# Kernel tuning notes

Hardware: AMD Instinct MI355X
Metric: run time of the kernel (lower is better)

The kernel has to match this reference:

```python
import jax, jax.numpy as jnp
import numpy as np

N = 65536   # num nodes
F = 512     # input feature dim
H = 256     # hid_dim
E = 1048576 # num edges (avg degree 16)
R = 512     # num_reps


def setup_inputs() -> dict:
    key = jax.random.key(0)
    ks = jax.random.split(key, 8)
    nodes = jax.random.normal(ks[0], (N, F), dtype=jnp.float32)
    c_nodes = jax.random.normal(ks[1], (N, F), dtype=jnp.float32)  # corrupted features
    senders = jax.random.randint(ks[2], (E,), 0, N, dtype=jnp.int32)
    receivers = jax.random.randint(ks[3], (E,), 0, N, dtype=jnp.int32)
    s = 1.0 / np.sqrt(F)
    W = jax.random.uniform(ks[4], (F, H), jnp.float32, -s, s)  # Dense kernel
    b = jnp.zeros((H,), jnp.float32)                            # Dense bias
    W_bilinear = jax.random.normal(ks[5], (H, H), jnp.float32) / np.sqrt(H)
    centers = jax.random.normal(ks[6], (R, H), jnp.float32)     # EucCluster param
    return dict(nodes=nodes, c_nodes=c_nodes, senders=senders, receivers=receivers,
                W=W, b=b, W_bilinear=W_bilinear, centers=centers)


def _gcn(x, senders, receivers, W, b):
    # jraph.GraphConvolution(Dense, add_self_edges=False, symmetric_normalization=True)
    x = x @ W + b  # [N,H]
    ones = jnp.ones((senders.shape[0],), x.dtype)
    deg_s = jax.ops.segment_sum(ones, senders, num_segments=N)
    x = x * jax.lax.rsqrt(jnp.maximum(deg_s, 1.0))[:, None]
    x = jax.ops.segment_sum(x[senders], receivers, num_segments=N)  # scatter-sum aggregation
    deg_r = jax.ops.segment_sum(ones, receivers, num_segments=N)
    x = x * jax.lax.rsqrt(jnp.maximum(deg_r, 1.0))[:, None]
    return jax.nn.selu(x)  # activation 'SeLU'


def reference(nodes, c_nodes, senders, receivers, W, b, W_bilinear, centers):
    # DGI with shared single-layer GCN (train=False path; single layer => no dropout)
    nodes1 = _gcn(nodes, senders, receivers, W, b)    # [N,H]
    nodes2 = _gcn(c_nodes, senders, receivers, W, b)  # [N,H]
    summary = jax.nn.sigmoid(jnp.mean(nodes1, axis=0))  # dgi_readout, [H]
    all_nodes = jnp.concatenate([nodes1, nodes2], axis=0)  # [2N,H]
    logits = (all_nodes @ W_bilinear) @ summary  # bilinear, [2N]
    # row L2-normalize embeddings
    emb = nodes1 / jnp.linalg.norm(nodes1, axis=1, keepdims=True)
    # Euclidean clustering: pairwise dists via GEMM trick
    d2 = (jnp.sum(emb * emb, axis=1)[:, None]
          + jnp.sum(centers * centers, axis=1)[None, :]
          - 2.0 * emb @ centers.T)  # [N,R]
    dists = jnp.sqrt(jnp.maximum(d2, 1e-12))
    cluster_dists = jnp.min(dists, axis=1)   # per-node dist to nearest center
    rep_ids = jnp.argmin(dists, axis=0)      # representative node per center
    cluster_loss = jnp.sum(cluster_dists)
    return emb, centers, rep_ids, cluster_loss, logits
```

## Files before the change

kernel.cpp:

```cpp
#include <hip/hip_runtime.h>
#include <math.h>

#define N_NODES 65536
#define F_DIM 512
#define H_DIM 256
#define E_EDGES 1048576
#define R_REPS 512

typedef _Float16 f16x8 __attribute__((ext_vector_type(8)));
typedef float f32x4_t __attribute__((ext_vector_type(4)));

__device__ __forceinline__ float selu_f(float x) {
    const float SC = 1.0507009873554804934f;
    const float AL = 1.6732632423543772848f;
    return x > 0.f ? SC * x : SC * AL * expm1f(x);
}

__device__ __forceinline__ void split8(const float* __restrict__ g, f16x8* hi, f16x8* lo) {
    float4 v0 = *(const float4*)g;
    float4 v1 = *(const float4*)(g + 4);
    f16x8 h, l;
    h[0] = (_Float16)v0.x; h[1] = (_Float16)v0.y; h[2] = (_Float16)v0.z; h[3] = (_Float16)v0.w;
    h[4] = (_Float16)v1.x; h[5] = (_Float16)v1.y; h[6] = (_Float16)v1.z; h[7] = (_Float16)v1.w;
    l[0] = (_Float16)(v0.x - (float)h[0]); l[1] = (_Float16)(v0.y - (float)h[1]);
    l[2] = (_Float16)(v0.z - (float)h[2]); l[3] = (_Float16)(v0.w - (float)h[3]);
    l[4] = (_Float16)(v1.x - (float)h[4]); l[5] = (_Float16)(v1.y - (float)h[5]);
    l[6] = (_Float16)(v1.z - (float)h[6]); l[7] = (_Float16)(v1.w - (float)h[7]);
    *hi = h; *lo = l;
}

__device__ __forceinline__ int wave_sort64(int v, int lane) {
    #pragma unroll
    for (int k = 2; k <= 64; k <<= 1) {
        #pragma unroll
        for (int j = k >> 1; j > 0; j >>= 1) {
            int p = __shfl_xor(v, j);
            bool takeMin = (((lane & j) == 0) == ((lane & k) == 0));
            int mn = min(v, p), mx = max(v, p);
            v = takeMin ? mn : mx;
        }
    }
    return v;
}

__global__ void k_init(int* cnt_s, int* cnt_r, float* colsum,
                       unsigned* node_min, unsigned long long* center_min,
                       double* loss_acc) {
    int i = blockIdx.x * 256 + threadIdx.x;
    if (i < N_NODES) { cnt_s[i] = 0; cnt_r[i] = 0; node_min[i] = 0x7F800000u; }
    if (i < H_DIM) colsum[i] = 0.f;
    if (i < R_REPS) center_min[i] = ~0ull;
    if (i == 0) *loss_acc = 0.0;
}

__global__ void k_degree(const int* __restrict__ senders, const int* __restrict__ receivers,
                         int* __restrict__ cnt_s, int* __restrict__ cnt_r) {
    int e = blockIdx.x * 256 + threadIdx.x;
    if (e < E_EDGES) {
        atomicAdd(&cnt_s[senders[e]], 1);
        atomicAdd(&cnt_r[receivers[e]], 1);
    }
}

__global__ void k_invsqrt(const int* __restrict__ cnt_s, const int* __restrict__ cnt_r,
                          float* __restrict__ inv_s, float* __restrict__ inv_r) {
    int i = blockIdx.x * 256 + threadIdx.x;
    if (i < N_NODES) {
        inv_s[i] = 1.0f / sqrtf(fmaxf((float)cnt_s[i], 1.f));
        inv_r[i] = 1.0f / sqrtf(fmaxf((float)cnt_r[i], 1.f));
    }
}

__global__ __launch_bounds__(1024) void k_scan(const int* __restrict__ cnt,
                                               int* __restrict__ row_ptr,
                                               int* __restrict__ cursor) {
    __shared__ int part[1024];
    int t = threadIdx.x;
    int base = t * 64;
    int s = 0;
    #pragma unroll 8
    for (int i = 0; i < 64; ++i) s += cnt[base + i];
    part[t] = s;
    __syncthreads();
    for (int off = 1; off < 1024; off <<= 1) {
        int other = (t >= off) ? part[t - off] : 0;
        __syncthreads();
        part[t] += other;
        __syncthreads();
    }
    int run = part[t] - s;
    for (int i = 0; i < 64; ++i) {
        row_ptr[base + i] = run;
        cursor[base + i] = run;
        run += cnt[base + i];
    }
    if (t == 1023) row_ptr[N_NODES] = run;
}

__global__ void k_fill(const int* __restrict__ senders, const int* __restrict__ receivers,
                       int* __restrict__ cursor, int* __restrict__ csr_send) {
    int e = blockIdx.x * 256 + threadIdx.x;
    if (e < E_EDGES) {
        int pos = atomicAdd(&cursor[receivers[e]], 1);
        csr_send[pos] = senders[e];
    }
}

__global__ void k_splitWT(const float* __restrict__ W, _Float16* __restrict__ hiT,
                          _Float16* __restrict__ loT) {
    int idx = blockIdx.x * 256 + threadIdx.x;
    int n = idx & (H_DIM - 1);
    int k = idx >> 8;
    float x = W[(size_t)k * H_DIM + n];
    _Float16 h = (_Float16)x;
    hiT[(size_t)n * F_DIM + k] = h;
    loT[(size_t)n * F_DIM + k] = (_Float16)(x - (float)h);
}

#define MFMA3(accv, AH, AL, BH, BL) \
    accv = __builtin_amdgcn_mfma_f32_16x16x32_f16(AH, BH, accv, 0, 0, 0); \
    accv = __builtin_amdgcn_mfma_f32_16x16x32_f16(AH, BL, accv, 0, 0, 0); \
    accv = __builtin_amdgcn_mfma_f32_16x16x32_f16(AL, BH, accv, 0, 0, 0);

#define MFMA_CORE \
    f16x8 ah[4], al[4]; \
    _Pragma("unroll") \
    for (int mi = 0; mi < 4; ++mi) { \
        ah[mi] = *(f16x8*)&Ah[wm * 64 + mi * 16 + lrow][kg * 8]; \
        al[mi] = *(f16x8*)&Al[wm * 64 + mi * 16 + lrow][kg * 8]; \
    } \
    _Pragma("unroll") \
    for (int ni = 0; ni < 4; ++ni) { \
        f16x8 bh = *(f16x8*)&Bh[wn * 64 + ni * 16 + lrow][kg * 8]; \
        f16x8 bl = *(f16x8*)&Bl[wn * 64 + ni * 16 + lrow][kg * 8]; \
        _Pragma("unroll") \
        for (int mi = 0; mi < 4; ++mi) { MFMA3(acc[mi][ni], ah[mi], al[mi], bh, bl) } \
    }

#define STAGE_A_F32(gA) { \
    f16x8 h0, l0, h1, l1; \
    split8((gA) + k0, &h0, &l0); \
    split8((gA) + k0 + 8, &h1, &l1); \
    *(f16x8*)&Ah[sr][skh] = h0; *(f16x8*)&Ah[sr][skh + 8] = h1; \
    *(f16x8*)&Al[sr][skh] = l0; *(f16x8*)&Al[sr][skh + 8] = l1; }

#define STAGE_B_F32(gB) { \
    f16x8 h0, l0, h1, l1; \
    split8((gB) + k0, &h0, &l0); \
    split8((gB) + k0 + 8, &h1, &l1); \
    *(f16x8*)&Bh[sr][skh] = h0; *(f16x8*)&Bh[sr][skh + 8] = h1; \
    *(f16x8*)&Bl[sr][skh] = l0; *(f16x8*)&Bl[sr][skh + 8] = l1; }

__global__ __launch_bounds__(256) void k_gemm_mfma(
    const float* __restrict__ A,
    const _Float16* __restrict__ BThi, const _Float16* __restrict__ BTlo,
    const float* __restrict__ bias, const float* __restrict__ inv_s,
    float* __restrict__ X, int K) {
    __shared__ _Float16 Ah[128][40], Al[128][40], Bh[128][40], Bl[128][40];
    const int t = threadIdx.x;
    const int lane = t & 63;
    const int wm = (t >> 6) >> 1, wn = (t >> 6) & 1;
    const int lrow = lane & 15, kg = lane >> 4;
    const int m0 = blockIdx.x * 128, n0 = blockIdx.y * 128;
    const int sr = t >> 1, skh = (t & 1) << 4;
    const float* gA = A + (size_t)(m0 + sr) * K + skh;
    const _Float16* gBh = BThi + (size_t)(n0 + sr) * K + skh;
    const _Float16* gBl = BTlo + (size_t)(n0 + sr) * K + skh;
    f32x4_t acc[4][4] = {};
    for (int k0 = 0; k0 < K; k0 += 32) {
        __syncthreads();
        STAGE_A_F32(gA)
        *(float4*)&Bh[sr][skh]     = *(const float4*)(gBh + k0);
        *(float4*)&Bh[sr][skh + 8] = *(const float4*)(gBh + k0 + 8);
        *(float4*)&Bl[sr][skh]     = *(const float4*)(gBl + k0);
        *(float4*)&Bl[sr][skh + 8] = *(const float4*)(gBl + k0 + 8);
        __syncthreads();
        MFMA_CORE
    }
    #pragma unroll
    for (int ni = 0; ni < 4; ++ni) {
        int col = n0 + wn * 64 + ni * 16 + lrow;
        float bc = bias[col];
        #pragma unroll
        for (int mi = 0; mi < 4; ++mi) {
            #pragma unroll
            for (int j = 0; j < 4; ++j) {
                int row = m0 + wm * 64 + mi * 16 + kg * 4 + j;
                X[(size_t)row * H_DIM + col] = (acc[mi][ni][j] + bc) * inv_s[row];
            }
        }
    }
}

__global__ __launch_bounds__(256) void k_cluster_mfma(
    const float* __restrict__ emb, const float* __restrict__ centers,
    const float* __restrict__ e2, const float* __restrict__ c2,
    unsigned* __restrict__ node_min, unsigned long long* __restrict__ center_min) {
    __shared__ _Float16 Ah[128][40], Al[128][40], Bh[128][40], Bl[128][40];
    __shared__ unsigned s_nmin[128];
    __shared__ unsigned long long s_cmin[128];
    const int t = threadIdx.x;
    const int lane = t & 63;
    const int wm = (t >> 6) >> 1, wn = (t >> 6) & 1;
    const int lrow = lane & 15, kg = lane >> 4;
    const int m0 = blockIdx.x * 128, n0 = blockIdx.y * 128;
    const int sr = t >> 1, skh = (t & 1) << 4;
    const int K = H_DIM;
    const float* gA = emb + (size_t)(m0 + sr) * K + skh;
    const float* gB = centers + (size_t)(n0 + sr) * K + skh;
    if (t < 128) { s_nmin[t] = 0x7F800000u; s_cmin[t] = ~0ull; }
    f32x4_t acc[4][4] = {};
    for (int k0 = 0; k0 < K; k0 += 32) {
        __syncthreads();
        STAGE_A_F32(gA)
        STAGE_B_F32(gB)
        __syncthreads();
        MFMA_CORE
    }
    float cv[4];
    #pragma unroll
    for (int ni = 0; ni < 4; ++ni) cv[ni] = c2[n0 + wn * 64 + ni * 16 + lrow];
    unsigned long long cb[4] = {~0ull, ~0ull, ~0ull, ~0ull};
    #pragma unroll
    for (int mi = 0; mi < 4; ++mi) {
        #pragma unroll
        for (int j = 0; j < 4; ++j) {
            int lr = wm * 64 + mi * 16 + kg * 4 + j;
            int row = m0 + lr;
            float ev = e2[row];
            float rmin = 3.402823466e+38f;
            #pragma unroll
            for (int ni = 0; ni < 4; ++ni) {
                float d2 = ev + cv[ni] - 2.f * acc[mi][ni][j];
                float d = sqrtf(fmaxf(d2, 1e-12f));
                rmin = fminf(rmin, d);
                unsigned long long pk = ((unsigned long long)__float_as_uint(d) << 32) | (unsigned)row;
                if (pk < cb[ni]) cb[ni] = pk;
            }
            atomicMin(&s_nmin[lr], __float_as_uint(rmin));
        }
    }
    #pragma unroll
    for (int ni = 0; ni < 4; ++ni)
        atomicMin(&s_cmin[wn * 64 + ni * 16 + lrow], cb[ni]);
    __syncthreads();
    if (t < 128) {
        atomicMin(&node_min[m0 + t], s_nmin[t]);
        atomicMin(&center_min[n0 + t], s_cmin[t]);
    }
}

__global__ __launch_bounds__(256) void k_agg1(
    const float* __restrict__ X, const int* __restrict__ csr_send,
    const int* __restrict__ row_ptr, const float* __restrict__ inv_r,
    float* __restrict__ out_emb) {
    int node = blockIdx.x * 4 + (threadIdx.x >> 6);
    int lane = threadIdx.x & 63;
    int beg = row_ptr[node], end = row_ptr[node + 1];
    float4 acc = {0.f, 0.f, 0.f, 0.f};
    for (int b = beg; b < end; b += 64) {
        int n = min(64, end - b);
        int myS = (lane < n) ? csr_send[b + lane] : 0x7FFFFFFF;
        myS = wave_sort64(myS, lane);
        for (int i = 0; i < n; ++i) {
            int s = __shfl(myS, i);
            float4 x = *(const float4*)&X[(size_t)s * H_DIM + (lane << 2)];
            acc.x += x.x; acc.y += x.y; acc.z += x.z; acc.w += x.w;
        }
    }
    float ir = inv_r[node];
    float4 o;
    o.x = selu_f(acc.x * ir);
    o.y = selu_f(acc.y * ir);
    o.z = selu_f(acc.z * ir);
    o.w = selu_f(acc.w * ir);
    *(float4*)&out_emb[(size_t)node * H_DIM + (lane << 2)] = o;
}

__global__ __launch_bounds__(256) void k_agg2(
    const float* __restrict__ X, const int* __restrict__ csr_send,
    const int* __restrict__ row_ptr, const float* __restrict__ inv_r,
    const float* __restrict__ v, float* __restrict__ out) {
    int node = blockIdx.x * 4 + (threadIdx.x >> 6);
    int lane = threadIdx.x & 63;
    int beg = row_ptr[node], end = row_ptr[node + 1];
    float4 acc = {0.f, 0.f, 0.f, 0.f};
    for (int b = beg; b < end; b += 64) {
        int n = min(64, end - b);
        int myS = (lane < n) ? csr_send[b + lane] : 0x7FFFFFFF;
        myS = wave_sort64(myS, lane);
        for (int i = 0; i < n; ++i) {
            int s = __shfl(myS, i);
            float4 x = *(const float4*)&X[(size_t)s * H_DIM + (lane << 2)];
            acc.x += x.x; acc.y += x.y; acc.z += x.z; acc.w += x.w;
        }
    }
    float ir = inv_r[node];
    float4 vv = *(const float4*)&v[lane << 2];
    float d = selu_f(acc.x * ir) * vv.x + selu_f(acc.y * ir) * vv.y
            + selu_f(acc.z * ir) * vv.z + selu_f(acc.w * ir) * vv.w;
    #pragma unroll
    for (int off = 32; off; off >>= 1) d += __shfl_down(d, off);
    if (lane == 0) out[node] = d;
}

__global__ __launch_bounds__(256) void k_colsum(const float* __restrict__ nodes1,
                                                float* __restrict__ colsum) {
    int t = threadIdx.x;
    size_t r0 = (size_t)blockIdx.x * 64;
    float s = 0.f;
    for (int r = 0; r < 64; ++r) s += nodes1[(r0 + r) * H_DIM + t];
    atomicAdd(&colsum[t], s);
}

__global__ void k_summary_v(const float* __restrict__ colsum, const float* __restrict__ Wb,
                            float* __restrict__ v) {
    __shared__ float s_sum[H_DIM];
    int t = threadIdx.x;
    float m = colsum[t] * (1.f / (float)N_NODES);
    s_sum[t] = 1.f / (1.f + expf(-m));
    __syncthreads();
    float acc = 0.f;
    for (int j = 0; j < H_DIM; ++j) acc += Wb[t * H_DIM + j] * s_sum[j];
    v[t] = acc;
}

__global__ __launch_bounds__(256) void k_normrow(
    float* __restrict__ emb, const float* __restrict__ v,
    float* __restrict__ logits, float* __restrict__ e2) {
    int row = blockIdx.x * 4 + (threadIdx.x >> 6);
    int lane = threadIdx.x & 63;
    float4 a = *(float4*)&emb[(size_t)row * H_DIM + (lane << 2)];
    float4 vv = *(const float4*)&v[lane << 2];
    float d = a.x * vv.x + a.y * vv.y + a.z * vv.z + a.w * vv.w;
    float ss = a.x * a.x + a.y * a.y + a.z * a.z + a.w * a.w;
    #pragma unroll
    for (int off = 32; off; off >>= 1) {
        d += __shfl_xor(d, off);
        ss += __shfl_xor(ss, off);
    }
    if (lane == 0) logits[row] = d;
    float inv = 1.f / sqrtf(ss);
    a.x *= inv; a.y *= inv; a.z *= inv; a.w *= inv;
    *(float4*)&emb[(size_t)row * H_DIM + (lane << 2)] = a;
    float s2 = a.x * a.x + a.y * a.y + a.z * a.z + a.w * a.w;
    #pragma unroll
    for (int off = 32; off; off >>= 1) s2 += __shfl_xor(s2, off);
    if (lane == 0) e2[row] = s2;
}

__global__ __launch_bounds__(256) void k_c2(const float* __restrict__ centers,
                                            float* __restrict__ c2) {
    int row = blockIdx.x * 4 + (threadIdx.x >> 6);
    int lane = threadIdx.x & 63;
    float4 a = *(const float4*)&centers[(size_t)row * H_DIM + (lane << 2)];
    float ss = a.x * a.x + a.y * a.y + a.z * a.z + a.w * a.w;
    #pragma unroll
    for (int off = 32; off; off >>= 1) ss += __shfl_xor(ss, off);
    if (lane == 0) c2[row] = ss;
}

__global__ __launch_bounds__(256) void k_loss(const unsigned* __restrict__ node_min,
                                              double* __restrict__ acc) {
    int i = blockIdx.x * 256 + threadIdx.x;
    float s = __uint_as_float(node_min[i]);
    #pragma unroll
    for (int off = 32; off; off >>= 1) s += __shfl_down(s, off);
    __shared__ float ws[4];
    int lane = threadIdx.x & 63, w = threadIdx.x >> 6;
    if (lane == 0) ws[w] = s;
    __syncthreads();
    if (threadIdx.x == 0) {
        float tot = ws[0] + ws[1] + ws[2] + ws[3];
        atomicAdd(acc, (double)tot);
    }
}

__global__ void k_finalize(const unsigned long long* __restrict__ center_min,
                           const double* __restrict__ loss_acc,
                           float* __restrict__ rep_out, float* __restrict__ loss_out) {
    int t = blockIdx.x * 256 + threadIdx.x;
    if (t < R_REPS) rep_out[t] = (float)(unsigned)(center_min[t] & 0xFFFFFFFFull);
    if (t == 0) *loss_out = (float)(*loss_acc);
}

extern "C" void kernel_launch(void* const* d_in, const int* in_sizes, int n_in,
                              void* d_out, int out_size, void* d_ws, size_t ws_size,
                              hipStream_t stream) {
    const float* nodes   = (const float*)d_in[0];
    const float* c_nodes = (const float*)d_in[1];
    const int* senders   = (const int*)d_in[2];
    const int* receivers = (const int*)d_in[3];
    const float* W       = (const float*)d_in[4];
    const float* bias    = (const float*)d_in[5];
    const float* Wb      = (const float*)d_in[6];
    const float* centers = (const float*)d_in[7];

    float* out = (float*)d_out;
    float* out_emb    = out;
    float* out_cent   = out + (size_t)N_NODES * H_DIM;
    float* out_rep    = out_cent + (size_t)R_REPS * H_DIM;
    float* out_loss   = out_rep + R_REPS;
    float* out_logits = out_loss + 1;

    char* wp = (char*)d_ws;
    unsigned long long* center_min = (unsigned long long*)wp; wp += (size_t)R_REPS * 8;
    double* loss_acc = (double*)wp;             wp += 8;
    float* X = (float*)wp;                      wp += (size_t)N_NODES * H_DIM * 4;
    int* csr_send = (int*)wp;                   wp += (size_t)E_EDGES * 4;
    int* row_ptr = (int*)wp;                    wp += (size_t)(N_NODES + 2) * 4;
    int* cursor = (int*)wp;                     wp += (size_t)N_NODES * 4;
    int* cnt_s = (int*)wp;                      wp += (size_t)N_NODES * 4;
    int* cnt_r = (int*)wp;                      wp += (size_t)N_NODES * 4;
    float* inv_s = (float*)wp;                  wp += (size_t)N_NODES * 4;
    float* inv_r = (float*)wp;                  wp += (size_t)N_NODES * 4;
    float* colsum = (float*)wp;                 wp += (size_t)H_DIM * 4;
    float* v = (float*)wp;                      wp += (size_t)H_DIM * 4;
    float* e2 = (float*)wp;                     wp += (size_t)N_NODES * 4;
    float* c2 = (float*)wp;                     wp += (size_t)R_REPS * 4;
    unsigned* node_min = (unsigned*)wp;         wp += (size_t)N_NODES * 4;
    _Float16* WhiT = (_Float16*)wp;             wp += (size_t)H_DIM * F_DIM * 2;
    _Float16* WloT = (_Float16*)wp;             wp += (size_t)H_DIM * F_DIM * 2;

    k_init<<<N_NODES / 256, 256, 0, stream>>>(cnt_s, cnt_r, colsum, node_min, center_min, loss_acc);
    k_degree<<<E_EDGES / 256, 256, 0, stream>>>(senders, receivers, cnt_s, cnt_r);
    k_invsqrt<<<N_NODES / 256, 256, 0, stream>>>(cnt_s, cnt_r, inv_s, inv_r);
    k_scan<<<1, 1024, 0, stream>>>(cnt_r, row_ptr, cursor);
    k_fill<<<E_EDGES / 256, 256, 0, stream>>>(senders, receivers, cursor, csr_send);
    k_splitWT<<<(F_DIM * H_DIM) / 256, 256, 0, stream>>>(W, WhiT, WloT);

    dim3 gg(N_NODES / 128, H_DIM / 128);
    k_gemm_mfma<<<gg, 256, 0, stream>>>(nodes, WhiT, WloT, bias, inv_s, X, F_DIM);
    k_agg1<<<N_NODES / 4, 256, 0, stream>>>(X, csr_send, row_ptr, inv_r, out_emb);

    k_colsum<<<N_NODES / 64, 256, 0, stream>>>(out_emb, colsum);
    k_summary_v<<<1, 256, 0, stream>>>(colsum, Wb, v);
    k_normrow<<<N_NODES / 4, 256, 0, stream>>>(out_emb, v, out_logits, e2);
    k_c2<<<R_REPS / 4, 256, 0, stream>>>(centers, c2);

    dim3 gc(N_NODES / 128, R_REPS / 128);
    k_cluster_mfma<<<gc, 256, 0, stream>>>(out_emb, centers, e2, c2, node_min, center_min);
    k_loss<<<N_NODES / 256, 256, 0, stream>>>(node_min, loss_acc);
    k_finalize<<<2, 256, 0, stream>>>(center_min, loss_acc, out_rep, out_loss);
    hipMemcpyAsync(out_cent, centers, (size_t)R_REPS * H_DIM * 4, hipMemcpyDeviceToDevice, stream);

    k_gemm_mfma<<<gg, 256, 0, stream>>>(c_nodes, WhiT, WloT, bias, inv_s, X, F_DIM);
    k_agg2<<<N_NODES / 4, 256, 0, stream>>>(X, csr_send, row_ptr, inv_r, v, out_logits + N_NODES);
}
```

Measured before the change: 902.2 us.

## Load GEMM B operands directly from global, batch both feature GEMMs

The two MFMA GEMM kernels no longer stage the B operand (split fp16 weights or centers) through shared memory. Each lane reads its fragments straight from global/L2, which halves LDS traffic and footprint per block. Centers are pre-split into hi/lo fp16 once, instead of being split per tile. Both node-feature GEMMs now run in one launch via blockIdx.z into separate buffers, and the grid is reordered so consecutive blocks share A rows. The cost is an extra N×H workspace buffer and uncoalesced, latency-exposed global loads for B inside the MFMA loop.

```diff
diff --git a/kernel.cpp b/kernel.cpp
--- a/kernel.cpp
+++ b/kernel.cpp
@@ -8,6 +8,7 @@
 #define R_REPS 512
 
 typedef _Float16 f16x8 __attribute__((ext_vector_type(8)));
+typedef _Float16 f16x4 __attribute__((ext_vector_type(4)));
 typedef float f32x4_t __attribute__((ext_vector_type(4)));
 
 __device__ __forceinline__ float selu_f(float x) {
@@ -117,12 +118,40 @@
     loT[(size_t)n * F_DIM + k] = (_Float16)(x - (float)h);
 }
 
+__global__ void k_split(const float* __restrict__ src, _Float16* __restrict__ hi,
+                        _Float16* __restrict__ lo, int n4) {
+    int i = blockIdx.x * 256 + threadIdx.x;
+    if (i >= n4) return;
+    float4 v = ((const float4*)src)[i];
+    f16x4 h, l;
+    h[0] = (_Float16)v.x; h[1] = (_Float16)v.y; h[2] = (_Float16)v.z; h[3] = (_Float16)v.w;
+    l[0] = (_Float16)(v.x - (float)h[0]);
+    l[1] = (_Float16)(v.y - (float)h[1]);
+    l[2] = (_Float16)(v.z - (float)h[2]);
+    l[3] = (_Float16)(v.w - (float)h[3]);
+    ((f16x4*)hi)[i] = h;
+    ((f16x4*)lo)[i] = l;
+}
+
 #define MFMA3(accv, AH, AL, BH, BL) \
     accv = __builtin_amdgcn_mfma_f32_16x16x32_f16(AH, BH, accv, 0, 0, 0); \
     accv = __builtin_amdgcn_mfma_f32_16x16x32_f16(AH, BL, accv, 0, 0, 0); \
     accv = __builtin_amdgcn_mfma_f32_16x16x32_f16(AL, BH, accv, 0, 0, 0);
 
-#define MFMA_CORE \
+#define STAGE_A_F32(gA) { \
+    f16x8 h0, l0, h1, l1; \
+    split8((gA) + k0, &h0, &l0); \
+    split8((gA) + k0 + 8, &h1, &l1); \
+    *(f16x8*)&Ah[sr][skh] = h0; *(f16x8*)&Ah[sr][skh + 8] = h1; \
+    *(f16x8*)&Al[sr][skh] = l0; *(f16x8*)&Al[sr][skh + 8] = l1; }
+
+#define MFMA_CORE_BDIRECT(gBh, gBl, K) \
+    f16x8 bh[4], bl[4]; \
+    _Pragma("unroll") \
+    for (int ni = 0; ni < 4; ++ni) { \
+        bh[ni] = *(const f16x8*)((gBh) + (size_t)ni * 16 * (K) + k0); \
+        bl[ni] = *(const f16x8*)((gBl) + (size_t)ni * 16 * (K) + k0); \
+    } \
     f16x8 ah[4], al[4]; \
     _Pragma("unroll") \
     for (int mi = 0; mi < 4; ++mi) { \
@@ -130,52 +159,34 @@
         al[mi] = *(f16x8*)&Al[wm * 64 + mi * 16 + lrow][kg * 8]; \
     } \
     _Pragma("unroll") \
-    for (int ni = 0; ni < 4; ++ni) { \
-        f16x8 bh = *(f16x8*)&Bh[wn * 64 + ni * 16 + lrow][kg * 8]; \
-        f16x8 bl = *(f16x8*)&Bl[wn * 64 + ni * 16 + lrow][kg * 8]; \
+    for (int ni = 0; ni < 4; ++ni) \
         _Pragma("unroll") \
-        for (int mi = 0; mi < 4; ++mi) { MFMA3(acc[mi][ni], ah[mi], al[mi], bh, bl) } \
-    }
-
-#define STAGE_A_F32(gA) { \
-    f16x8 h0, l0, h1, l1; \
-    split8((gA) + k0, &h0, &l0); \
-    split8((gA) + k0 + 8, &h1, &l1); \
-    *(f16x8*)&Ah[sr][skh] = h0; *(f16x8*)&Ah[sr][skh + 8] = h1; \
-    *(f16x8*)&Al[sr][skh] = l0; *(f16x8*)&Al[sr][skh + 8] = l1; }
-
-#define STAGE_B_F32(gB) { \
-    f16x8 h0, l0, h1, l1; \
-    split8((gB) + k0, &h0, &l0); \
-    split8((gB) + k0 + 8, &h1, &l1); \
-    *(f16x8*)&Bh[sr][skh] = h0; *(f16x8*)&Bh[sr][skh + 8] = h1; \
-    *(f16x8*)&Bl[sr][skh] = l0; *(f16x8*)&Bl[sr][skh + 8] = l1; }
+        for (int mi = 0; mi < 4; ++mi) { MFMA3(acc[mi][ni], ah[mi], al[mi], bh[ni], bl[ni]) }
 
 __global__ __launch_bounds__(256) void k_gemm_mfma(
-    const float* __restrict__ A,
+    const float* __restrict__ A0, const float* __restrict__ A1,
     const _Float16* __restrict__ BThi, const _Float16* __restrict__ BTlo,
     const float* __restrict__ bias, const float* __restrict__ inv_s,
-    float* __restrict__ X, int K) {
-    __shared__ _Float16 Ah[128][40], Al[128][40], Bh[128][40], Bl[128][40];
+    float* __restrict__ X0, float* __restrict__ X1) {
+    __shared__ _Float16 Ah[128][40], Al[128][40];
     const int t = threadIdx.x;
     const int lane = t & 63;
     const int wm = (t >> 6) >> 1, wn = (t >> 6) & 1;
     const int lrow = lane & 15, kg = lane >> 4;
-    const int m0 = blockIdx.x * 128, n0 = blockIdx.y * 128;
+    const int n0 = blockIdx.x * 128, m0 = blockIdx.y * 128;
+    const int K = F_DIM;
+    const float* A = blockIdx.z ? A1 : A0;
+    float* X = blockIdx.z ? X1 : X0;
     const int sr = t >> 1, skh = (t & 1) << 4;
     const float* gA = A + (size_t)(m0 + sr) * K + skh;
-    const _Float16* gBh = BThi + (size_t)(n0 + sr) * K + skh;
-    const _Float16* gBl = BTlo + (size_t)(n0 + sr) * K + skh;
+    const _Float16* gBh = BThi + (size_t)(n0 + wn * 64 + lrow) * K + kg * 8;
+    const _Float16* gBl = BTlo + (size_t)(n0 + wn * 64 + lrow) * K + kg * 8;
     f32x4_t acc[4][4] = {};
     for (int k0 = 0; k0 < K; k0 += 32) {
         __syncthreads();
         STAGE_A_F32(gA)
-        *(float4*)&Bh[sr][skh]     = *(const float4*)(gBh + k0);
-        *(float4*)&Bh[sr][skh + 8] = *(const float4*)(gBh + k0 + 8);
-        *(float4*)&Bl[sr][skh]     = *(const float4*)(gBl + k0);
-        *(float4*)&Bl[sr][skh + 8] = *(const float4*)(gBl + k0 + 8);
-        __syncthreads();
-        MFMA_CORE
+        __syncthreads();
+        MFMA_CORE_BDIRECT(gBh, gBl, K)
     }
     #pragma unroll
     for (int ni = 0; ni < 4; ++ni) {
@@ -193,29 +204,30 @@
 }
 
 __global__ __launch_bounds__(256) void k_cluster_mfma(
-    const float* __restrict__ emb, const float* __restrict__ centers,
+    const float* __restrict__ emb,
+    const _Float16* __restrict__ Chi, const _Float16* __restrict__ Clo,
     const float* __restrict__ e2, const float* __restrict__ c2,
     unsigned* __restrict__ node_min, unsigned long long* __restrict__ center_min) {
-    __shared__ _Float16 Ah[128][40], Al[128][40], Bh[128][40], Bl[128][40];
+    __shared__ _Float16 Ah[128][40], Al[128][40];
     __shared__ unsigned s_nmin[128];
     __shared__ unsigned long long s_cmin[128];
     const int t = threadIdx.x;
     const int lane = t & 63;
     const int wm = (t >> 6) >> 1, wn = (t >> 6) & 1;
     const int lrow = lane & 15, kg = lane >> 4;
-    const int m0 = blockIdx.x * 128, n0 = blockIdx.y * 128;
+    const int n0 = blockIdx.x * 128, m0 = blockIdx.y * 128;
+    const int K = H_DIM;
     const int sr = t >> 1, skh = (t & 1) << 4;
-    const int K = H_DIM;
     const float* gA = emb + (size_t)(m0 + sr) * K + skh;
-    const float* gB = centers + (size_t)(n0 + sr) * K + skh;
+    const _Float16* gBh = Chi + (size_t)(n0 + wn * 64 + lrow) * K + kg * 8;
+    const _Float16* gBl = Clo + (size_t)(n0 + wn * 64 + lrow) * K + kg * 8;
     if (t < 128) { s_nmin[t] = 0x7F800000u; s_cmin[t] = ~0ull; }
     f32x4_t acc[4][4] = {};
     for (int k0 = 0; k0 < K; k0 += 32) {
         __syncthreads();
         STAGE_A_F32(gA)
-        STAGE_B_F32(gB)
-        __syncthreads();
-        MFMA_CORE
+        __syncthreads();
+        MFMA_CORE_BDIRECT(gBh, gBl, K)
     }
     float cv[4];
     #pragma unroll
@@ -407,6 +419,7 @@
     unsigned long long* center_min = (unsigned long long*)wp; wp += (size_t)R_REPS * 8;
     double* loss_acc = (double*)wp;             wp += 8;
     float* X = (float*)wp;                      wp += (size_t)N_NODES * H_DIM * 4;
+    float* X2 = (float*)wp;                     wp += (size_t)N_NODES * H_DIM * 4;
     int* csr_send = (int*)wp;                   wp += (size_t)E_EDGES * 4;
     int* row_ptr = (int*)wp;                    wp += (size_t)(N_NODES + 2) * 4;
     int* cursor = (int*)wp;                     wp += (size_t)N_NODES * 4;
@@ -421,6 +434,8 @@
     unsigned* node_min = (unsigned*)wp;         wp += (size_t)N_NODES * 4;
     _Float16* WhiT = (_Float16*)wp;             wp += (size_t)H_DIM * F_DIM * 2;
     _Float16* WloT = (_Float16*)wp;             wp += (size_t)H_DIM * F_DIM * 2;
+    _Float16* Chi = (_Float16*)wp;              wp += (size_t)R_REPS * H_DIM * 2;
+    _Float16* Clo = (_Float16*)wp;              wp += (size_t)R_REPS * H_DIM * 2;
 
     k_init<<<N_NODES / 256, 256, 0, stream>>>(cnt_s, cnt_r, colsum, node_min, center_min, loss_acc);
     k_degree<<<E_EDGES / 256, 256, 0, stream>>>(senders, receivers, cnt_s, cnt_r);
@@ -428,9 +443,10 @@
     k_scan<<<1, 1024, 0, stream>>>(cnt_r, row_ptr, cursor);
     k_fill<<<E_EDGES / 256, 256, 0, stream>>>(senders, receivers, cursor, csr_send);
     k_splitWT<<<(F_DIM * H_DIM) / 256, 256, 0, stream>>>(W, WhiT, WloT);
-
-    dim3 gg(N_NODES / 128, H_DIM / 128);
-    k_gemm_mfma<<<gg, 256, 0, stream>>>(nodes, WhiT, WloT, bias, inv_s, X, F_DIM);
+    k_split<<<(R_REPS * H_DIM / 4) / 256, 256, 0, stream>>>(centers, Chi, Clo, R_REPS * H_DIM / 4);
+
+    dim3 gg(H_DIM / 128, N_NODES / 128, 2);
+    k_gemm_mfma<<<gg, 256, 0, stream>>>(nodes, c_nodes, WhiT, WloT, bias, inv_s, X, X2);
     k_agg1<<<N_NODES / 4, 256, 0, stream>>>(X, csr_send, row_ptr, inv_r, out_emb);
 
     k_colsum<<<N_NODES / 64, 256, 0, stream>>>(out_emb, colsum);
@@ -438,12 +454,11 @@
     k_normrow<<<N_NODES / 4, 256, 0, stream>>>(out_emb, v, out_logits, e2);
     k_c2<<<R_REPS / 4, 256, 0, stream>>>(centers, c2);
 
-    dim3 gc(N_NODES / 128, R_REPS / 128);
-    k_cluster_mfma<<<gc, 256, 0, stream>>>(out_emb, centers, e2, c2, node_min, center_min);
+    dim3 gc(R_REPS / 128, N_NODES / 128);
+    k_cluster_mfma<<<gc, 256, 0, stream>>>(out_emb, Chi, Clo, e2, c2, node_min, center_min);
     k_loss<<<N_NODES / 256, 256, 0, stream>>>(node_min, loss_acc);
     k_finalize<<<2, 256, 0, stream>>>(center_min, loss_acc, out_rep, out_loss);
     hipMemcpyAsync(out_cent, centers, (size_t)R_REPS * H_DIM * 4, hipMemcpyDeviceToDevice, stream);
 
-    k_gemm_mfma<<<gg, 256, 0, stream>>>(c_nodes, WhiT, WloT, bias, inv_s, X, F_DIM);
-    k_agg2<<<N_NODES / 4, 256, 0, stream>>>(X, csr_send, row_ptr, inv_r, v, out_logits + N_NODES);
-}
+    k_agg2<<<N_NODES / 4, 256, 0, stream>>>(X2, csr_send, row_ptr, inv_r, v, out_logits + N_NODES);
+}
```

Result: slower. 959.4 us (+6.3%).
